# Performance work log

Measured on AMD Instinct MI355X. Metric: run time of the kernel, lower is better.

Reference implementation:

```python
import jax, jax.numpy as jnp
import numpy as np


def setup_inputs() -> dict:
    key = jax.random.key(0)
    k1, k2 = jax.random.split(key)
    n, d, num_classes = 262144, 128, 512
    inputs = jax.random.normal(k1, (n, d), dtype=jnp.float32)
    targets = jax.random.randint(k2, (n,), 0, num_classes)
    return {"inputs": inputs, "targets": targets, "num_classes": num_classes}


def reference(inputs, targets, num_classes):
    beta = 0.1
    eps = 1e-12  # torch F.normalize default eps (norm clamped to min eps)
    # L2-normalize features
    x = inputs / jnp.maximum(jnp.linalg.norm(inputs, axis=1, keepdims=True), eps)  # [n, d]

    # Per-class centers: mean of normalized features, then L2-normalize, detached.
    ones = jnp.ones((x.shape[0],), dtype=x.dtype)
    counts = jax.ops.segment_sum(ones, targets, num_segments=num_classes)          # [C]
    csum = jax.ops.segment_sum(x, targets, num_segments=num_classes)               # [C, d]
    cmean = csum / jnp.maximum(counts, 1.0)[:, None]
    centers = cmean / jnp.maximum(jnp.linalg.norm(cmean, axis=1, keepdims=True), eps)
    centers = jax.lax.stop_gradient(centers)  # .detach() in original

    # Numerator logit: center of own class dotted with own feature
    pos = jnp.sum(centers[targets] * x, axis=1) / beta                             # [n]
    # Denominator: sum of exp over all *present* classes (original only builds
    # centers for pids that appear in the batch)
    scores = jnp.exp(centers @ x.T / beta)                                         # [C, n]
    present = counts > 0
    denom = jnp.sum(jnp.where(present[:, None], scores, 0.0), axis=0)              # [n]
    return -jnp.mean(pos - jnp.log(denom))
```

## Files before the change

### kernel.cpp

```cpp
#include <hip/hip_runtime.h>
#include <stdint.h>

#define NROWS 262144
#define DDIM 128
#define NCLS 512
#define NHB 64
constexpr float INV_BETA = 10.0f;
constexpr float EXP2_SCALE = 14.426950408889634f;

typedef __bf16 v8bf __attribute__((ext_vector_type(8)));
typedef float v4f __attribute__((ext_vector_type(4)));

__device__ inline unsigned short f2bf(float f) {
    uint32_t u = __builtin_bit_cast(uint32_t, f);
    u += 0x7FFFu + ((u >> 16) & 1u);
    return (unsigned short)(u >> 16);
}
__device__ inline float bflo(uint32_t u) { return __builtin_bit_cast(float, u << 16); }
__device__ inline float bfhi(uint32_t u) { return __builtin_bit_cast(float, u & 0xFFFF0000u); }

__global__ __launch_bounds__(256) void k1_normalize(
    const float* __restrict__ in, unsigned short* __restrict__ xb) {
    int t = threadIdx.x;
    int w = t >> 6;
    int half = (t & 63) >> 5;
    int lane32 = t & 31;
    int hw = blockIdx.x * 8 + w * 2 + half;
    int r0 = hw * 4;
    float4 v[4];
#pragma unroll
    for (int j = 0; j < 4; ++j)
        v[j] = *reinterpret_cast<const float4*>(in + (size_t)(r0 + j) * DDIM + lane32 * 4);
    float s[4];
#pragma unroll
    for (int j = 0; j < 4; ++j)
        s[j] = v[j].x * v[j].x + v[j].y * v[j].y + v[j].z * v[j].z + v[j].w * v[j].w;
#pragma unroll
    for (int off = 1; off < 32; off <<= 1) {
#pragma unroll
        for (int j = 0; j < 4; ++j) s[j] += __shfl_xor(s[j], off);
    }
#pragma unroll
    for (int j = 0; j < 4; ++j) {
        float iv = rsqrtf(fmaxf(s[j], 1e-24f));
        ushort4 o;
        o.x = f2bf(v[j].x * iv); o.y = f2bf(v[j].y * iv);
        o.z = f2bf(v[j].z * iv); o.w = f2bf(v[j].w * iv);
        *reinterpret_cast<ushort4*>(xb + (size_t)(r0 + j) * DDIM + lane32 * 4) = o;
    }
}

__global__ __launch_bounds__(256) void k_hist(
    const int* __restrict__ tgt, int* __restrict__ bh) {
    __shared__ int h[NCLS];
    int t = threadIdx.x;
    for (int i = t; i < NCLS; i += 256) h[i] = 0;
    __syncthreads();
    int base = blockIdx.x * (NROWS / NHB);
    for (int i = base + t; i < base + NROWS / NHB; i += 256)
        atomicAdd(&h[tgt[i]], 1);
    __syncthreads();
    for (int i = t; i < NCLS; i += 256)
        bh[blockIdx.x * NCLS + i] = h[i];
}

__global__ __launch_bounds__(512) void k_prefix(
    const int* __restrict__ bh, int* __restrict__ counts, int* __restrict__ offs,
    int* __restrict__ base, float* __restrict__ nabsG, float* __restrict__ out) {
    __shared__ int sc[NCLS];
    __shared__ int za;
    int t = threadIdx.x;
    int cnt = 0;
#pragma unroll 8
    for (int b = 0; b < NHB; ++b) cnt += bh[b * NCLS + t];
    counts[t] = cnt;
    sc[t] = cnt;
    if (t == 0) za = 0;
    __syncthreads();
    for (int off = 1; off < NCLS; off <<= 1) {
        int v = (t >= off) ? sc[t - off] : 0;
        __syncthreads();
        sc[t] += v;
        __syncthreads();
    }
    int excl = sc[t] - cnt;
    offs[t] = excl;
    if (cnt == 0) atomicAdd(&za, 1);
    int run = excl;
    for (int b = 0; b < NHB; ++b) {
        base[b * NCLS + t] = run;
        run += bh[b * NCLS + t];
    }
    __syncthreads();
    if (t == 0) { *nabsG = (float)za; *out = 0.0f; }
}

__global__ __launch_bounds__(256) void k_scatter(
    const int* __restrict__ tgt, const int* __restrict__ base, int* __restrict__ ridx) {
    __shared__ int cur[NCLS];
    int t = threadIdx.x;
    int b = blockIdx.x;
    cur[t] = base[b * NCLS + t];
    cur[t + 256] = base[b * NCLS + t + 256];
    __syncthreads();
    int r0 = b * (NROWS / NHB);
    for (int i = t; i < NROWS / NHB; i += 256) {
        int row = r0 + i;
        int c = tgt[row];
        int pos = atomicAdd(&cur[c], 1);
        ridx[pos] = row;
    }
}

__global__ __launch_bounds__(512) void k_centers(
    const unsigned short* __restrict__ xb, const int* __restrict__ ridx,
    const int* __restrict__ counts, const int* __restrict__ offs,
    unsigned short* __restrict__ cen, float* __restrict__ out) {
    __shared__ float2 sP[8][64];
    int t = threadIdx.x, w = t >> 6, l = t & 63;
    int cl = blockIdx.x;
    int cnt = counts[cl], start = offs[cl];
    const uint32_t* xb32 = (const uint32_t*)xb;
    float a0 = 0.0f, a1 = 0.0f;
    int per = (cnt + 7) >> 3;
    int lo = w * per, hi = min(cnt, lo + per);
    int i = lo;
    for (; i + 8 <= hi; i += 8) {
        int id[8]; uint32_t v[8];
#pragma unroll
        for (int j = 0; j < 8; ++j) id[j] = ridx[start + i + j];
#pragma unroll
        for (int j = 0; j < 8; ++j) v[j] = xb32[(size_t)id[j] * 64 + l];
#pragma unroll
        for (int j = 0; j < 8; ++j) { a0 += bflo(v[j]); a1 += bfhi(v[j]); }
    }
    for (; i < hi; ++i) {
        uint32_t v = xb32[(size_t)ridx[start + i] * 64 + l];
        a0 += bflo(v); a1 += bfhi(v);
    }
    sP[w][l] = make_float2(a0, a1);
    __syncthreads();
    if (w == 0) {
        float c0 = 0.0f, c1 = 0.0f;
#pragma unroll
        for (int q = 0; q < 8; ++q) { c0 += sP[q][l].x; c1 += sP[q][l].y; }
        float fc = fmaxf((float)cnt, 1.0f);
        c0 /= fc; c1 /= fc;
        float ss = c0 * c0 + c1 * c1;
        for (int off = 1; off < 64; off <<= 1) ss += __shfl_xor(ss, off);
        float inv = 1.0f / fmaxf(sqrtf(ss), 1e-12f);
        ushort2 o;
        o.x = f2bf(c0 * inv); o.y = f2bf(c1 * inv);
        *reinterpret_cast<ushort2*>(cen + (size_t)cl * DDIM + l * 2) = o;
        if (l == 0)
            atomicAdd(out, -(float)cnt * sqrtf(ss) * (INV_BETA / (float)NROWS));
    }
}

__global__ __launch_bounds__(1024) void k4_loss(
    const unsigned short* __restrict__ xb, const unsigned short* __restrict__ cen,
    const float* __restrict__ nabsG, float* __restrict__ out) {
    extern __shared__ char lds[];
    char* xL0 = lds;
    char* xL1 = lds + 32768;
    float* denP = (float*)(lds + 65536);
    float* wsum = (float*)(lds + 73728);
    int t = threadIdx.x, w = t >> 6, l = t & 63;
    int lm = l & 15, lk = l >> 4;
    float nabs = *nabsG;

    v8bf afr[2][4];
#pragma unroll
    for (int m = 0; m < 2; ++m)
#pragma unroll
        for (int kc = 0; kc < 4; ++kc) {
            int arow = w * 32 + m * 16 + lm;
            afr[m][kc] = *reinterpret_cast<const v8bf*>(cen + (size_t)arow * DDIM + kc * 32 + lk * 8);
        }

    int block0 = blockIdx.x * 1024;
    int srow = t >> 3;
    int sw = (srow & 7) << 4;
    int c16 = (t & 7) * 2;
    int dst0 = srow * 256 + ((c16 * 16) ^ sw);
    int dst1 = srow * 256 + (((c16 + 1) * 16) ^ sw);
    const char* xbB = (const char*)xb + (size_t)block0 * 256;

    uint4 r0 = *(const uint4*)(xbB + t * 32);
    uint4 r1 = *(const uint4*)(xbB + t * 32 + 16);
    *(uint4*)(xL0 + dst0) = r0;
    *(uint4*)(xL0 + dst1) = r1;
    float lossAcc = 0.0f;
    __syncthreads();

    for (int tile = 0; tile < 8; ++tile) {
        char* xc = (tile & 1) ? xL1 : xL0;
        char* xn = (tile & 1) ? xL0 : xL1;
        if (tile < 7) {
            const char* src = xbB + (size_t)(tile + 1) * 32768 + t * 32;
            r0 = *(const uint4*)(src);
            r1 = *(const uint4*)(src + 16);
        }

#pragma unroll
        for (int h = 0; h < 2; ++h) {
            v4f acc[2][4];
            v4f zero = {0.0f, 0.0f, 0.0f, 0.0f};
#pragma unroll
            for (int m = 0; m < 2; ++m)
#pragma unroll
                for (int n = 0; n < 4; ++n) acc[m][n] = zero;

#pragma unroll
            for (int kc = 0; kc < 4; ++kc) {
                int kb = kc * 64 + lk * 16;
                v8bf b[4];
#pragma unroll
                for (int n = 0; n < 4; ++n) {
                    int brow = h * 64 + n * 16 + lm;
                    b[n] = *reinterpret_cast<const v8bf*>(xc + brow * 256 + (kb ^ ((brow & 7) << 4)));
                }
#pragma unroll
                for (int m = 0; m < 2; ++m)
#pragma unroll
                    for (int n = 0; n < 4; ++n)
                        acc[m][n] = __builtin_amdgcn_mfma_f32_16x16x32_bf16(afr[m][kc], b[n], acc[m][n], 0, 0, 0);
            }

#pragma unroll
            for (int n = 0; n < 4; ++n) {
                float se = 0.0f;
#pragma unroll
                for (int m = 0; m < 2; ++m) {
#pragma unroll
                    for (int rr = 0; rr < 4; ++rr)
                        se += __builtin_amdgcn_exp2f(acc[m][n][rr] * EXP2_SCALE);
                }
                se += __shfl_xor(se, 16); se += __shfl_xor(se, 32);
                if (l < 16) denP[w * 128 + h * 64 + n * 16 + lm] = se;
            }
        }
        __syncthreads();
        if (tile < 7) {
            *(uint4*)(xn + dst0) = r0;
            *(uint4*)(xn + dst1) = r1;
        }
        if (t < 128) {
            float den = 0.0f;
#pragma unroll
            for (int q = 0; q < 16; ++q) den += denP[q * 128 + t];
            lossAcc += __logf(den - nabs);
        }
        __syncthreads();
    }
    if (t < 128) {
#pragma unroll
        for (int off = 1; off < 64; off <<= 1) lossAcc += __shfl_xor(lossAcc, off);
        if (l == 0) wsum[w] = lossAcc;
    }
    __syncthreads();
    if (t == 0) atomicAdd(out, (wsum[0] + wsum[1]) * (1.0f / NROWS));
}

extern "C" void kernel_launch(void* const* d_in, const int* in_sizes, int n_in,
                              void* d_out, int out_size, void* d_ws, size_t ws_size,
                              hipStream_t stream) {
    const float* in = (const float*)d_in[0];
    const int* tgt = (const int*)d_in[1];
    float* out = (float*)d_out;
    char* ws = (char*)d_ws;
    unsigned short* xb = (unsigned short*)(ws);
    int* counts = (int*)(ws + 67108864);
    int* offs = (int*)(ws + 67110912);
    float* nabsG = (float*)(ws + 67112960);
    unsigned short* cen = (unsigned short*)(ws + 67115264);
    int* ridx = (int*)(ws + 67246336);
    int* bh = (int*)(ws + 68294912);
    int* base = (int*)(ws + 68557056);

    (void)hipFuncSetAttribute((const void*)k4_loss,
                              hipFuncAttributeMaxDynamicSharedMemorySize, 73792);

    hipLaunchKernelGGL(k1_normalize, dim3(8192), dim3(256), 0, stream, in, xb);
    hipLaunchKernelGGL(k_hist, dim3(NHB), dim3(256), 0, stream, tgt, bh);
    hipLaunchKernelGGL(k_prefix, dim3(1), dim3(512), 0, stream, bh, counts, offs, base, nabsG, out);
    hipLaunchKernelGGL(k_scatter, dim3(NHB), dim3(256), 0, stream, tgt, base, ridx);
    hipLaunchKernelGGL(k_centers, dim3(NCLS), dim3(512), 0, stream, xb, ridx, counts, offs, cen, out);
    hipLaunchKernelGGL(k4_loss, dim3(256), dim3(1024), 73792, stream, xb, cen, nabsG, out);
}
```

Baseline: 115.6 us.

## Fuse histogram into normalize kernel and stream loss tiles via direct global-to-LDS loads

Merges the histogram kernel into the normalization launch as extra blocks, removing one kernel launch and letting the histogram run concurrently with normalization. In the loss kernel, the register-staged double-buffer copies are replaced with global_load_lds direct-to-LDS transfers, using a swizzle that is now applied on the global source side. This frees registers and removes the mid-tile LDS store step, but adds explicit vmcnt waits before each barrier.

```diff
diff --git a/kernel.cpp b/kernel.cpp
--- a/kernel.cpp
+++ b/kernel.cpp
@@ -19,9 +19,28 @@
 __device__ inline float bflo(uint32_t u) { return __builtin_bit_cast(float, u << 16); }
 __device__ inline float bfhi(uint32_t u) { return __builtin_bit_cast(float, u & 0xFFFF0000u); }
 
+#define GLL16(gsrc, ldst)                                                        \
+    __builtin_amdgcn_global_load_lds(                                            \
+        (const __attribute__((address_space(1))) void*)(uintptr_t)(gsrc),        \
+        (__attribute__((address_space(3))) void*)(uintptr_t)(ldst), 16, 0, 0)
+
 __global__ __launch_bounds__(256) void k1_normalize(
-    const float* __restrict__ in, unsigned short* __restrict__ xb) {
+    const float* __restrict__ in, const int* __restrict__ tgt,
+    unsigned short* __restrict__ xb, int* __restrict__ bh) {
+    __shared__ int h[NCLS];
     int t = threadIdx.x;
+    if (blockIdx.x >= 8192) {
+        int b = blockIdx.x - 8192;
+        for (int i = t; i < NCLS; i += 256) h[i] = 0;
+        __syncthreads();
+        int base = b * (NROWS / NHB);
+        for (int i = base + t; i < base + NROWS / NHB; i += 256)
+            atomicAdd(&h[tgt[i]], 1);
+        __syncthreads();
+        for (int i = t; i < NCLS; i += 256)
+            bh[b * NCLS + i] = h[i];
+        return;
+    }
     int w = t >> 6;
     int half = (t & 63) >> 5;
     int lane32 = t & 31;
@@ -48,20 +67,6 @@
         o.z = f2bf(v[j].z * iv); o.w = f2bf(v[j].w * iv);
         *reinterpret_cast<ushort4*>(xb + (size_t)(r0 + j) * DDIM + lane32 * 4) = o;
     }
-}
-
-__global__ __launch_bounds__(256) void k_hist(
-    const int* __restrict__ tgt, int* __restrict__ bh) {
-    __shared__ int h[NCLS];
-    int t = threadIdx.x;
-    for (int i = t; i < NCLS; i += 256) h[i] = 0;
-    __syncthreads();
-    int base = blockIdx.x * (NROWS / NHB);
-    for (int i = base + t; i < base + NROWS / NHB; i += 256)
-        atomicAdd(&h[tgt[i]], 1);
-    __syncthreads();
-    for (int i = t; i < NCLS; i += 256)
-        bh[blockIdx.x * NCLS + i] = h[i];
 }
 
 __global__ __launch_bounds__(512) void k_prefix(
@@ -179,27 +184,27 @@
         }
 
     int block0 = blockIdx.x * 1024;
-    int srow = t >> 3;
-    int sw = (srow & 7) << 4;
-    int c16 = (t & 7) * 2;
-    int dst0 = srow * 256 + ((c16 * 16) ^ sw);
-    int dst1 = srow * 256 + (((c16 + 1) * 16) ^ sw);
     const char* xbB = (const char*)xb + (size_t)block0 * 256;
 
-    uint4 r0 = *(const uint4*)(xbB + t * 32);
-    uint4 r1 = *(const uint4*)(xbB + t * 32 + 16);
-    *(uint4*)(xL0 + dst0) = r0;
-    *(uint4*)(xL0 + dst1) = r1;
+    int C0 = w * 128 + l;
+    int C1 = C0 + 64;
+    int so0 = (C0 >> 4) * 256 + ((((C0 & 15) ^ ((C0 >> 4) & 7))) << 4);
+    int so1 = (C1 >> 4) * 256 + ((((C1 & 15) ^ ((C1 >> 4) & 7))) << 4);
+    int dw = w * 2048;
+
+    GLL16(xbB + so0, xL0 + dw);
+    GLL16(xbB + so1, xL0 + dw + 1024);
     float lossAcc = 0.0f;
+    asm volatile("s_waitcnt vmcnt(0)" ::: "memory");
     __syncthreads();
 
     for (int tile = 0; tile < 8; ++tile) {
         char* xc = (tile & 1) ? xL1 : xL0;
         char* xn = (tile & 1) ? xL0 : xL1;
         if (tile < 7) {
-            const char* src = xbB + (size_t)(tile + 1) * 32768 + t * 32;
-            r0 = *(const uint4*)(src);
-            r1 = *(const uint4*)(src + 16);
+            const char* s = xbB + (size_t)(tile + 1) * 32768;
+            GLL16(s + so0, xn + dw);
+            GLL16(s + so1, xn + dw + 1024);
         }
 
 #pragma unroll
@@ -240,11 +245,8 @@
                 if (l < 16) denP[w * 128 + h * 64 + n * 16 + lm] = se;
             }
         }
-        __syncthreads();
-        if (tile < 7) {
-            *(uint4*)(xn + dst0) = r0;
-            *(uint4*)(xn + dst1) = r1;
-        }
+        asm volatile("s_waitcnt vmcnt(0)" ::: "memory");
+        __syncthreads();
         if (t < 128) {
             float den = 0.0f;
 #pragma unroll
@@ -281,8 +283,7 @@
     (void)hipFuncSetAttribute((const void*)k4_loss,
                               hipFuncAttributeMaxDynamicSharedMemorySize, 73792);
 
-    hipLaunchKernelGGL(k1_normalize, dim3(8192), dim3(256), 0, stream, in, xb);
-    hipLaunchKernelGGL(k_hist, dim3(NHB), dim3(256), 0, stream, tgt, bh);
+    hipLaunchKernelGGL(k1_normalize, dim3(8192 + NHB), dim3(256), 0, stream, in, tgt, xb, bh);
     hipLaunchKernelGGL(k_prefix, dim3(1), dim3(512), 0, stream, bh, counts, offs, base, nabsG, out);
     hipLaunchKernelGGL(k_scatter, dim3(NHB), dim3(256), 0, stream, tgt, base, ridx);
     hipLaunchKernelGGL(k_centers, dim3(NCLS), dim3(512), 0, stream, xb, ridx, counts, offs, cen, out);
```

After: 112.8 us. 1.02x faster.
